# Kernel tuning notes

Hardware: AMD Instinct MI355X
Metric: run time of the kernel (lower is better)

The kernel has to match this reference:

```python
import jax, jax.numpy as jnp
import numpy as np

B, C, H, W = 32, 1, 28, 896
WW = WS = 28
S = (W - WW) // WS + 1  # 32 windows
CONV_DIM, FC_DIM, NUM_CLASSES = 64, 128, 83
FC_IN = CONV_DIM * (H // 2) * (WW // 2)  # 64*14*14 = 12544


def setup_inputs() -> dict:
    key = jax.random.key(0)
    ks = jax.random.split(key, 9)
    sc = 0.05
    return {
        "x": jax.random.normal(ks[0], (B, C, H, W), jnp.float32),
        "conv1_w": jax.random.normal(ks[1], (CONV_DIM, C, 3, 3), jnp.float32) * sc,
        "conv1_b": jax.random.normal(ks[2], (CONV_DIM,), jnp.float32) * sc,
        "conv2_w": jax.random.normal(ks[3], (CONV_DIM, CONV_DIM, 3, 3), jnp.float32) * sc,
        "conv2_b": jax.random.normal(ks[4], (CONV_DIM,), jnp.float32) * sc,
        "fc1_w": jax.random.normal(ks[5], (FC_DIM, FC_IN), jnp.float32) * sc,
        "fc1_b": jax.random.normal(ks[6], (FC_DIM,), jnp.float32) * sc,
        "fc2_w": jax.random.normal(ks[7], (NUM_CLASSES, FC_DIM), jnp.float32) * sc,
        "fc2_b": jax.random.normal(ks[8], (NUM_CLASSES,), jnp.float32) * sc,
    }


def _conv_relu(x, w, b):
    # 3x3 conv, stride 1, padding 1 (torch Conv2d padding=1), then ReLU
    y = jax.lax.conv_general_dilated(
        x, w, window_strides=(1, 1), padding=((1, 1), (1, 1)),
        dimension_numbers=("NCHW", "OIHW", "NCHW"))
    return jax.nn.relu(y + b[None, :, None, None])


def reference(x, conv1_w, conv1_b, conv2_w, conv2_b, fc1_w, fc1_b, fc2_w, fc2_b):
    Bx = x.shape[0]
    # WS == WW -> non-overlapping windows; extract all S windows at once via reshape
    # (B, C, H, S*WW) -> (B*S, C, H, WW)
    win = x.reshape(Bx, C, H, S, WW).transpose(0, 3, 1, 2, 4).reshape(Bx * S, C, H, WW)
    h = _conv_relu(win, conv1_w, conv1_b)
    h = _conv_relu(h, conv2_w, conv2_b)
    # MaxPool2d(2)
    h = jax.lax.reduce_window(h, -jnp.inf, jax.lax.max,
                              window_dimensions=(1, 1, 2, 2),
                              window_strides=(1, 1, 2, 2), padding="VALID")
    # dropout is identity in eval mode
    h = h.reshape(Bx * S, FC_IN)  # torch.flatten(x, 1) on NCHW matches row-major reshape
    h = jax.nn.relu(h @ fc1_w.T + fc1_b)
    logits = h @ fc2_w.T + fc2_b  # (B*S, num_classes)
    # -> (B, num_classes, S) as in the torch module
    return logits.reshape(Bx, S, NUM_CLASSES).transpose(0, 2, 1)
```

## Files before the change

### kernel.cpp

```cpp
#include <hip/hip_runtime.h>
#include <hip/hip_bf16.h>


typedef __attribute__((ext_vector_type(8))) short short8;
typedef __attribute__((ext_vector_type(4))) float f32x4;
typedef __attribute__((ext_vector_type(16))) float f32x16;

#define WB1_E   0u
#define WB2_E   2048u
#define WFC1_E  38912u
#define WFC2_E  1644544u
#define POOL_E  1656832u
#define PART_B  29003776u

__device__ __forceinline__ unsigned short f2bf(float f) {
  unsigned u = __float_as_uint(f);
  u += 0x7fffu + ((u >> 16) & 1u);
  return (unsigned short)(u >> 16);
}
__device__ __forceinline__ unsigned cvtpk_bf16(float a, float b) {
  unsigned r;
  asm("v_cvt_pk_bf16_f32 %0, %1, %2" : "=v"(r) : "v"(a), "v"(b));
  return r;
}

__global__ __launch_bounds__(256) void prep_kernel(
    const float* __restrict__ w1, const float* __restrict__ c1b,
    const float* __restrict__ w2, const float* __restrict__ wfc1,
    const float* __restrict__ wfc2, unsigned short* __restrict__ ws16)
{
  int i = blockIdx.x * blockDim.x + threadIdx.x;
  if (i < 2048) {
    int j = i & 7, l = (i >> 3) & 63, nt = i >> 9;
    int n = nt * 16 + (l & 15), k = 8 * (l >> 4) + j;
    float v = (k < 9) ? w1[n * 9 + k] : (k == 9 ? c1b[n] : 0.f);
    ws16[WB1_E + i] = f2bf(v);
  } else if (i < 38912) {
    int i2 = i - 2048;
    int j = i2 & 7, l = (i2 >> 3) & 63, rest = i2 >> 9;
    int ks = rest % 36, nh = rest / 36;
    int co = nh * 32 + (l & 31);
    int k = ks * 16 + (l >> 5) * 8 + j;
    int dydx = k >> 6, ci = k & 63;
    ws16[WB2_E + i2] = f2bf(w2[co * 576 + ci * 9 + dydx]);
  } else if (i < 1644544) {
    int i2 = i - 38912;
    int j = i2 & 7, l = (i2 >> 3) & 63, rest = i2 >> 9;
    int ks = rest % 392, nt = rest / 392;
    int fcn = nt * 16 + (l & 15);
    int kp = ks * 32 + 8 * (l >> 4) + j;
    int co = kp & 63, r2 = kp >> 6;
    int oxp = r2 % 14, oyp = r2 / 14;
    ws16[WFC1_E + i2] = f2bf(wfc1[fcn * 12544 + co * 196 + oyp * 14 + oxp]);
  } else if (i < 1656832) {
    int i2 = i - 1644544;
    int j = i2 & 7, l = (i2 >> 3) & 63, rest = i2 >> 9;
    int ks = rest & 3, nt = rest >> 2;
    int cls = nt * 16 + (l & 15);
    int k = ks * 32 + 8 * (l >> 4) + j;
    float v = (cls < 83) ? wfc2[cls * 128 + k] : 0.f;
    ws16[WFC2_E + i2] = f2bf(v);
  }
}

__global__ __launch_bounds__(512, 4) void conv_kernel(
    const float* __restrict__ x, const float* __restrict__ c2b,
    unsigned short* __restrict__ ws16)
{
  extern __shared__ char smem[];
  unsigned short* xw = (unsigned short*)(smem + 77760);

  const int tid = threadIdx.x;
  const int wave = tid >> 6, lane = tid & 63;
  const int bid = blockIdx.x;
  const int n = bid >> 1, hf = bid & 1;
  const int rlo = hf ? 15 : 0;
  const int M1 = hf ? 364 : 476;
  const int T1 = hf ? 23 : 30;
  const int lr_off = hf ? -15 : 1;

  const short8* wb1 = (const short8*)(ws16 + WB1_E);
  unsigned short* poolg = ws16 + POOL_E + (unsigned)n * 12544u;

  short8 z8 = {0, 0, 0, 0, 0, 0, 0, 0};
  {
    short8* l8 = (short8*)smem;
    for (int idx = tid; idx < 4860; idx += 512) l8[idx] = z8;
    const float* xg = x + (n >> 5) * 25088 + (n & 31) * 28;
    for (int i = tid; i < 900; i += 512) {
      int yy = (i * 2185) >> 16;
      int xx = i - yy * 30;
      int iy = yy - 1, ix = xx - 1;
      bool inb = (iy >= 0) && (iy < 28) && (ix >= 0) && (ix < 28);
      float v = inb ? xg[iy * 896 + ix] : 0.f;
      xw[i] = f2bf(v);
    }
  }
  __syncthreads();

  {
    const int g = lane >> 4, l15 = lane & 15;
    short8 b1f[4];
#pragma unroll
    for (int nt = 0; nt < 4; ++nt) b1f[nt] = wb1[nt * 64 + lane];
    for (int mt = wave; mt < T1; mt += 8) {
      int m = mt * 16 + l15;
      bool mval = m < M1;
      int mc = mval ? m : M1 - 1;
      int yr = (mc * 2341) >> 16;
      int rr = rlo + yr;
      int ox = mc - yr * 28;
      const char* xb = (const char*)xw + (rr * 30 + ox) * 2;
      short8 a = z8;
      if (g == 0) {
        a[0] = *(const short*)(xb + 0);
        a[1] = *(const short*)(xb + 2);
        a[2] = *(const short*)(xb + 4);
        a[3] = *(const short*)(xb + 60);
        a[4] = *(const short*)(xb + 62);
        a[5] = *(const short*)(xb + 64);
        a[6] = *(const short*)(xb + 120);
        a[7] = *(const short*)(xb + 122);
      } else if (g == 1) {
        a[0] = *(const short*)(xb + 124);
        a[1] = (short)0x3F80;
      }
      f32x4 d[4];
#pragma unroll
      for (int nt = 0; nt < 4; ++nt) {
        f32x4 zz = {0.f, 0.f, 0.f, 0.f};
        d[nt] = __builtin_amdgcn_mfma_f32_16x16x32_bf16(b1f[nt], a, zz, 0, 0, 0);
      }
      if (mval) {
        int spB = ((rr + lr_off) * 30 + ox + 1) * 144;
#pragma unroll
        for (int nt = 0; nt < 4; ++nt) {
          float r0 = fmaxf(d[nt][0], 0.f), r1 = fmaxf(d[nt][1], 0.f);
          float r2 = fmaxf(d[nt][2], 0.f), r3 = fmaxf(d[nt][3], 0.f);
          int co2 = nt * 16 + 4 * g;
          *(unsigned*)(smem + (spB + co2 * 2)) = cvtpk_bf16(r0, r1);
          *(unsigned*)(smem + (spB + co2 * 2 + 4)) = cvtpk_bf16(r2, r3);
        }
      }
    }
  }
  __syncthreads();

  {
    const int l31 = lane & 31;
    const int h = lane >> 5;
    const int T32 = hf ? 11 : 14;
    const int Wh  = hf ? 84 : 112;
    const float bias0 = c2b[l31];
    const float bias1 = c2b[32 + l31];
    const short8* wb2w = (const short8*)(ws16 + WB2_E) + lane;

    const bool v1 = (wave + 8) < T32;
    int baseB0, baseB1;
    {
      int lw = wave * 8 + (l31 >> 2);
      int py = lw / 14, px = lw % 14;
      baseB0 = ((2 * py + ((l31 >> 1) & 1)) * 30 + 2 * px + (l31 & 1)) * 144 + h * 16;
      int tI1 = v1 ? (wave + 8) : wave;
      int lw1 = tI1 * 8 + (l31 >> 2);
      int py1 = lw1 / 14, px1 = lw1 % 14;
      baseB1 = ((2 * py1 + ((l31 >> 1) & 1)) * 30 + 2 * px1 + (l31 & 1)) * 144 + h * 16;
    }
    f32x16 acc00 = (f32x16)(0.0f), acc01 = (f32x16)(0.0f);
    f32x16 acc10 = (f32x16)(0.0f), acc11 = (f32x16)(0.0f);

    short8 bfA0, bfA1, bfA2, bfA3;
    short8 bfB0, bfB1, bfB2, bfB3;

#define LOADB(d0, d1, d2, d3, hp) do {                                   \
      const int ph_ = (hp) >> 1, k0_ = ((hp) & 1) * 2;                   \
      d0 = wb2w[(ph_ * 4 + k0_) * 64];                                   \
      d1 = wb2w[(ph_ * 4 + k0_ + 1) * 64];                               \
      d2 = wb2w[2304 + (ph_ * 4 + k0_) * 64];                            \
      d3 = wb2w[2304 + (ph_ * 4 + k0_ + 1) * 64];                        \
    } while (0)
#define COMPT(hp, base, aL, aH, b0, b1, b2, b3) do {                     \
      const int ph_ = (hp) >> 1, k0_ = ((hp) & 1) * 2;                   \
      const int cell_ = ((ph_ / 3) * 30 + (ph_ % 3)) * 144 + 32 * k0_;   \
      short8 a0 = *(const short8*)(smem + (base + cell_));               \
      short8 a1 = *(const short8*)(smem + (base + cell_ + 32));          \
      aL = __builtin_amdgcn_mfma_f32_32x32x16_bf16(a0, b0, aL, 0, 0, 0); \
      aH = __builtin_amdgcn_mfma_f32_32x32x16_bf16(a0, b2, aH, 0, 0, 0); \
      aL = __builtin_amdgcn_mfma_f32_32x32x16_bf16(a1, b1, aL, 0, 0, 0); \
      aH = __builtin_amdgcn_mfma_f32_32x32x16_bf16(a1, b3, aH, 0, 0, 0); \
    } while (0)

    LOADB(bfA0, bfA1, bfA2, bfA3, 0);
    if (v1) {
#pragma unroll
      for (int hp = 0; hp < 18; hp += 2) {
        __builtin_amdgcn_s_barrier();
        if (hp + 1 < 18) LOADB(bfB0, bfB1, bfB2, bfB3, hp + 1);
        COMPT(hp, baseB0, acc00, acc01, bfA0, bfA1, bfA2, bfA3);
        COMPT(hp, baseB1, acc10, acc11, bfA0, bfA1, bfA2, bfA3);
        if (hp + 2 < 18) LOADB(bfA0, bfA1, bfA2, bfA3, hp + 2);
        COMPT(hp + 1, baseB0, acc00, acc01, bfB0, bfB1, bfB2, bfB3);
        COMPT(hp + 1, baseB1, acc10, acc11, bfB0, bfB1, bfB2, bfB3);
      }
    } else {
#pragma unroll
      for (int hp = 0; hp < 18; hp += 2) {
        __builtin_amdgcn_s_barrier();
        if (hp + 1 < 18) LOADB(bfB0, bfB1, bfB2, bfB3, hp + 1);
        COMPT(hp, baseB0, acc00, acc01, bfA0, bfA1, bfA2, bfA3);
        if (hp + 2 < 18) LOADB(bfA0, bfA1, bfA2, bfA3, hp + 2);
        COMPT(hp + 1, baseB0, acc00, acc01, bfB0, bfB1, bfB2, bfB3);
      }
    }
#undef LOADB
#undef COMPT

#pragma unroll
    for (int q = 0; q < 4; ++q) {
      int lw0 = wave * 8 + 2 * q + h;
      {
        float p0 = fmaxf(fmaxf(acc00[4 * q], acc00[4 * q + 1]),
                         fmaxf(acc00[4 * q + 2], acc00[4 * q + 3]));
        float p1 = fmaxf(fmaxf(acc01[4 * q], acc01[4 * q + 1]),
                         fmaxf(acc01[4 * q + 2], acc01[4 * q + 3]));
        unsigned pk = cvtpk_bf16(fmaxf(p0 + bias0, 0.f), fmaxf(p1 + bias1, 0.f));
        poolg[(hf * 112 + lw0) * 64 + l31]      = (unsigned short)pk;
        poolg[(hf * 112 + lw0) * 64 + 32 + l31] = (unsigned short)(pk >> 16);
      }
      if (v1) {
        int lw1 = (wave + 8) * 8 + 2 * q + h;
        if (lw1 < Wh) {
          float p0 = fmaxf(fmaxf(acc10[4 * q], acc10[4 * q + 1]),
                           fmaxf(acc10[4 * q + 2], acc10[4 * q + 3]));
          float p1 = fmaxf(fmaxf(acc11[4 * q], acc11[4 * q + 1]),
                           fmaxf(acc11[4 * q + 2], acc11[4 * q + 3]));
          unsigned pk = cvtpk_bf16(fmaxf(p0 + bias0, 0.f), fmaxf(p1 + bias1, 0.f));
          poolg[(hf * 112 + lw1) * 64 + l31]      = (unsigned short)pk;
          poolg[(hf * 112 + lw1) * 64 + 32 + l31] = (unsigned short)(pk >> 16);
        }
      }
    }
  }
}

__global__ __launch_bounds__(512) void fc1_kernel(unsigned short* __restrict__ ws16)
{
  extern __shared__ char smem[];
  short8* A8 = (short8*)smem;
  const int tid = threadIdx.x;
  const int wave = tid >> 6, lane = tid & 63;
  const int g = lane >> 4, l15 = lane & 15;
  const int ig = blockIdx.x >> 2, q = blockIdx.x & 3;
  const short8* pool8 = (const short8*)(ws16 + POOL_E);
  const short8* wf1 = (const short8*)(ws16 + WFC1_E);
  {
    int img = tid >> 5, l32 = tid & 31;
    const short8* src = pool8 + (ig * 16 + img) * 1568 + q * 392;
#pragma unroll
    for (int j = 0; j < 13; ++j) {
      int idx = l32 + 32 * j;
      if (idx < 392) A8[img * 393 + idx] = src[idx];
    }
  }
  __syncthreads();
  f32x4 accA = {0.f, 0.f, 0.f, 0.f}, accB = {0.f, 0.f, 0.f, 0.f};
  const short8* wbase = wf1 + (wave * 392 + q * 98) * 64 + lane;
  short8 bP0 = wbase[0 * 64], bP1 = wbase[1 * 64];
  short8 bP2 = wbase[2 * 64], bP3 = wbase[3 * 64];
#pragma unroll 1
  for (int c = 0; c < 24; ++c) {
    int ks = 4 * c;
    short8 a;
    a = A8[l15 * 393 + (ks + 0) * 4 + g];
    accA = __builtin_amdgcn_mfma_f32_16x16x32_bf16(a, bP0, accA, 0, 0, 0);
    bP0 = wbase[(ks + 4) * 64];
    a = A8[l15 * 393 + (ks + 1) * 4 + g];
    accB = __builtin_amdgcn_mfma_f32_16x16x32_bf16(a, bP1, accB, 0, 0, 0);
    bP1 = wbase[(ks + 5) * 64];
    a = A8[l15 * 393 + (ks + 2) * 4 + g];
    accA = __builtin_amdgcn_mfma_f32_16x16x32_bf16(a, bP2, accA, 0, 0, 0);
    bP2 = wbase[(ks + 6) * 64];
    a = A8[l15 * 393 + (ks + 3) * 4 + g];
    accB = __builtin_amdgcn_mfma_f32_16x16x32_bf16(a, bP3, accB, 0, 0, 0);
    bP3 = wbase[(ks + 7) * 64];
  }
  {
    short8 a;
    a = A8[l15 * 393 + 96 * 4 + g];
    accA = __builtin_amdgcn_mfma_f32_16x16x32_bf16(a, bP0, accA, 0, 0, 0);
    a = A8[l15 * 393 + 97 * 4 + g];
    accB = __builtin_amdgcn_mfma_f32_16x16x32_bf16(a, bP1, accB, 0, 0, 0);
  }
  _Float16* part = (_Float16*)((char*)ws16 + PART_B);
  int base = ((q * 64 + ig) * 16 + 4 * g) * 128 + wave * 16 + l15;
#pragma unroll
  for (int i = 0; i < 4; ++i) part[base + i * 128] = (_Float16)(accA[i] + accB[i]);
}

__global__ __launch_bounds__(512) void fc2_kernel(
    const float* __restrict__ b1, const float* __restrict__ b2,
    const unsigned short* __restrict__ ws16, float* __restrict__ out)
{
  __shared__ unsigned short h_s[16 * 136];
  const int tid = threadIdx.x;
  const int wave = tid >> 6, lane = tid & 63;
  const int g = lane >> 4, l15 = lane & 15;
  const int ig = blockIdx.x;
  const _Float16* part = (const _Float16*)((const char*)ws16 + PART_B);
#pragma unroll
  for (int t = 0; t < 4; ++t) {
    int u = tid + 512 * t;
    int img = u >> 7, fcn = u & 127;
    float s = 0.f;
#pragma unroll
    for (int q2 = 0; q2 < 4; ++q2)
      s += (float)part[((q2 * 64 + ig) * 16 + img) * 128 + fcn];
    h_s[img * 136 + fcn] = f2bf(fmaxf(s + b1[fcn], 0.f));
  }
  __syncthreads();
  if (wave < 6) {
    const short8* wf2 = (const short8*)(ws16 + WFC2_E);
    const short8* h8 = (const short8*)h_s;
    f32x4 a2 = {0.f, 0.f, 0.f, 0.f};
#pragma unroll
    for (int ks = 0; ks < 4; ++ks) {
      short8 b = wf2[(wave * 4 + ks) * 64 + lane];
      short8 a = h8[l15 * 17 + ks * 4 + g];
      a2 = __builtin_amdgcn_mfma_f32_16x16x32_bf16(a, b, a2, 0, 0, 0);
    }
    int cls = wave * 16 + l15;
    if (cls < 83) {
      float bias2 = b2[cls];
#pragma unroll
      for (int i = 0; i < 4; ++i) {
        int nimg = ig * 16 + 4 * g + i;
        out[((nimg >> 5) * 83 + cls) * 32 + (nimg & 31)] = a2[i] + bias2;
      }
    }
  }
}

extern "C" void kernel_launch(void* const* d_in, const int* in_sizes, int n_in,
                              void* d_out, int out_size, void* d_ws, size_t ws_size,
                              hipStream_t stream)
{
  const float* x    = (const float*)d_in[0];
  const float* w1   = (const float*)d_in[1];
  const float* c1b  = (const float*)d_in[2];
  const float* w2   = (const float*)d_in[3];
  const float* c2b  = (const float*)d_in[4];
  const float* wfc1 = (const float*)d_in[5];
  const float* bfc1 = (const float*)d_in[6];
  const float* wfc2 = (const float*)d_in[7];
  const float* bfc2 = (const float*)d_in[8];
  unsigned short* ws16 = (unsigned short*)d_ws;
  float* out = (float*)d_out;

  prep_kernel<<<6472, 256, 0, stream>>>(w1, c1b, w2, wfc1, wfc2, ws16);
  conv_kernel<<<2048, 512, 79616, stream>>>(x, c2b, ws16);
  fc1_kernel<<<256, 512, 100608, stream>>>(ws16);
  fc2_kernel<<<64, 512, 0, stream>>>(bfc1, bfc2, ws16, out);
}
```

Before: 95.07 us.

## Split conv work into quarter-image blocks and halve fc1 row tiles

The conv kernel now splits each window image into four pooled-row bands instead of two halves, with a smaller halo-padded LDS buffer and one accumulator tile per wave. The goal is more blocks and higher occupancy (launch bounds 6, about 44KB LDS). The cost is recomputing halo rows of conv1 and leaving idle waves that only join barriers. fc1 now handles 8 images per block across twice as many blocks, with smaller LDS, so half the MFMA rows are wasted duplicates.

```diff
diff --git a/kernel.cpp b/kernel.cpp
--- a/kernel.cpp
+++ b/kernel.cpp
@@ -63,21 +63,26 @@
   }
 }
 
-__global__ __launch_bounds__(512, 4) void conv_kernel(
+__global__ __launch_bounds__(512, 6) void conv_kernel(
     const float* __restrict__ x, const float* __restrict__ c2b,
     unsigned short* __restrict__ ws16)
 {
   extern __shared__ char smem[];
-  unsigned short* xw = (unsigned short*)(smem + 77760);
+  unsigned short* xw = (unsigned short*)(smem + 43200);
 
   const int tid = threadIdx.x;
   const int wave = tid >> 6, lane = tid & 63;
   const int bid = blockIdx.x;
-  const int n = bid >> 1, hf = bid & 1;
-  const int rlo = hf ? 15 : 0;
-  const int M1 = hf ? 364 : 476;
-  const int T1 = hf ? 23 : 30;
-  const int lr_off = hf ? -15 : 1;
+  const int n = bid >> 2, q = bid & 3;
+  const int p0 = (q == 0) ? 0 : (q == 1) ? 4 : (q == 2) ? 8 : 11;
+  const int PR = (q < 2) ? 4 : 3;
+  const int rlo = 2 * p0 - 1;
+  const int rstart = (q == 0) ? 0 : rlo;
+  const int rend = (rlo + 9 < 27) ? rlo + 9 : 27;
+  const int M1 = (rend - rstart + 1) * 28;
+  const int T1 = (M1 + 15) >> 4;
+  const int Wq = PR * 14;
+  const int Tq = (Wq + 7) >> 3;
 
   const short8* wb1 = (const short8*)(ws16 + WB1_E);
   unsigned short* poolg = ws16 + POOL_E + (unsigned)n * 12544u;
@@ -85,12 +90,12 @@
   short8 z8 = {0, 0, 0, 0, 0, 0, 0, 0};
   {
     short8* l8 = (short8*)smem;
-    for (int idx = tid; idx < 4860; idx += 512) l8[idx] = z8;
+    for (int idx = tid; idx < 2700; idx += 512) l8[idx] = z8;
     const float* xg = x + (n >> 5) * 25088 + (n & 31) * 28;
-    for (int i = tid; i < 900; i += 512) {
-      int yy = (i * 2185) >> 16;
-      int xx = i - yy * 30;
-      int iy = yy - 1, ix = xx - 1;
+    for (int i = tid; i < 360; i += 512) {
+      int xr = (i * 2185) >> 16;
+      int xx = i - xr * 30;
+      int iy = rlo - 1 + xr, ix = xx - 1;
       bool inb = (iy >= 0) && (iy < 28) && (ix >= 0) && (ix < 28);
       float v = inb ? xg[iy * 896 + ix] : 0.f;
       xw[i] = f2bf(v);
@@ -108,9 +113,9 @@
       bool mval = m < M1;
       int mc = mval ? m : M1 - 1;
       int yr = (mc * 2341) >> 16;
-      int rr = rlo + yr;
+      int rr = rstart + yr;
       int ox = mc - yr * 28;
-      const char* xb = (const char*)xw + (rr * 30 + ox) * 2;
+      const char* xb = (const char*)xw + ((rr - rlo) * 30 + ox) * 2;
       short8 a = z8;
       if (g == 0) {
         a[0] = *(const short*)(xb + 0);
@@ -132,7 +137,7 @@
         d[nt] = __builtin_amdgcn_mfma_f32_16x16x32_bf16(b1f[nt], a, zz, 0, 0, 0);
       }
       if (mval) {
-        int spB = ((rr + lr_off) * 30 + ox + 1) * 144;
+        int spB = ((rr - rlo) * 30 + ox + 1) * 144;
 #pragma unroll
         for (int nt = 0; nt < 4; ++nt) {
           float r0 = fmaxf(d[nt][0], 0.f), r1 = fmaxf(d[nt][1], 0.f);
@@ -149,28 +154,20 @@
   {
     const int l31 = lane & 31;
     const int h = lane >> 5;
-    const int T32 = hf ? 11 : 14;
-    const int Wh  = hf ? 84 : 112;
+    const bool real = wave < Tq;
+    const int tile = real ? wave : 0;
     const float bias0 = c2b[l31];
     const float bias1 = c2b[32 + l31];
     const short8* wb2w = (const short8*)(ws16 + WB2_E) + lane;
 
-    const bool v1 = (wave + 8) < T32;
-    int baseB0, baseB1;
-    {
-      int lw = wave * 8 + (l31 >> 2);
-      int py = lw / 14, px = lw % 14;
-      baseB0 = ((2 * py + ((l31 >> 1) & 1)) * 30 + 2 * px + (l31 & 1)) * 144 + h * 16;
-      int tI1 = v1 ? (wave + 8) : wave;
-      int lw1 = tI1 * 8 + (l31 >> 2);
-      int py1 = lw1 / 14, px1 = lw1 % 14;
-      baseB1 = ((2 * py1 + ((l31 >> 1) & 1)) * 30 + 2 * px1 + (l31 & 1)) * 144 + h * 16;
-    }
-    f32x16 acc00 = (f32x16)(0.0f), acc01 = (f32x16)(0.0f);
-    f32x16 acc10 = (f32x16)(0.0f), acc11 = (f32x16)(0.0f);
-
-    short8 bfA0, bfA1, bfA2, bfA3;
-    short8 bfB0, bfB1, bfB2, bfB3;
+    int lwl = tile * 8 + (l31 >> 2);
+    if (lwl >= Wq) lwl = Wq - 1;
+    int pyl = (lwl * 2341) >> 15;
+    int pxl = lwl - pyl * 14;
+    int p = l31 & 3;
+    const int baseB = ((2 * pyl + (p >> 1)) * 30 + 2 * pxl + (p & 1)) * 144 + h * 16;
+
+    f32x16 acc0 = (f32x16)(0.0f), acc1 = (f32x16)(0.0f);
 
 #define LOADB(d0, d1, d2, d3, hp) do {                                   \
       const int ph_ = (hp) >> 1, k0_ = ((hp) & 1) * 2;                   \
@@ -179,64 +176,50 @@
       d2 = wb2w[2304 + (ph_ * 4 + k0_) * 64];                            \
       d3 = wb2w[2304 + (ph_ * 4 + k0_ + 1) * 64];                        \
     } while (0)
-#define COMPT(hp, base, aL, aH, b0, b1, b2, b3) do {                     \
+#define COMPT(hp, b0, b1, b2, b3) do {                                   \
       const int ph_ = (hp) >> 1, k0_ = ((hp) & 1) * 2;                   \
       const int cell_ = ((ph_ / 3) * 30 + (ph_ % 3)) * 144 + 32 * k0_;   \
-      short8 a0 = *(const short8*)(smem + (base + cell_));               \
-      short8 a1 = *(const short8*)(smem + (base + cell_ + 32));          \
-      aL = __builtin_amdgcn_mfma_f32_32x32x16_bf16(a0, b0, aL, 0, 0, 0); \
-      aH = __builtin_amdgcn_mfma_f32_32x32x16_bf16(a0, b2, aH, 0, 0, 0); \
-      aL = __builtin_amdgcn_mfma_f32_32x32x16_bf16(a1, b1, aL, 0, 0, 0); \
-      aH = __builtin_amdgcn_mfma_f32_32x32x16_bf16(a1, b3, aH, 0, 0, 0); \
+      short8 a0 = *(const short8*)(smem + (baseB + cell_));              \
+      short8 a1 = *(const short8*)(smem + (baseB + cell_ + 32));         \
+      acc0 = __builtin_amdgcn_mfma_f32_32x32x16_bf16(a0, b0, acc0, 0, 0, 0); \
+      acc1 = __builtin_amdgcn_mfma_f32_32x32x16_bf16(a0, b2, acc1, 0, 0, 0); \
+      acc0 = __builtin_amdgcn_mfma_f32_32x32x16_bf16(a1, b1, acc0, 0, 0, 0); \
+      acc1 = __builtin_amdgcn_mfma_f32_32x32x16_bf16(a1, b3, acc1, 0, 0, 0); \
     } while (0)
 
-    LOADB(bfA0, bfA1, bfA2, bfA3, 0);
-    if (v1) {
+    if (real) {
+      short8 bfA0, bfA1, bfA2, bfA3, bfB0, bfB1, bfB2, bfB3;
+      LOADB(bfA0, bfA1, bfA2, bfA3, 0);
 #pragma unroll
       for (int hp = 0; hp < 18; hp += 2) {
         __builtin_amdgcn_s_barrier();
-        if (hp + 1 < 18) LOADB(bfB0, bfB1, bfB2, bfB3, hp + 1);
-        COMPT(hp, baseB0, acc00, acc01, bfA0, bfA1, bfA2, bfA3);
-        COMPT(hp, baseB1, acc10, acc11, bfA0, bfA1, bfA2, bfA3);
+        LOADB(bfB0, bfB1, bfB2, bfB3, hp + 1);
+        COMPT(hp, bfA0, bfA1, bfA2, bfA3);
         if (hp + 2 < 18) LOADB(bfA0, bfA1, bfA2, bfA3, hp + 2);
-        COMPT(hp + 1, baseB0, acc00, acc01, bfB0, bfB1, bfB2, bfB3);
-        COMPT(hp + 1, baseB1, acc10, acc11, bfB0, bfB1, bfB2, bfB3);
+        COMPT(hp + 1, bfB0, bfB1, bfB2, bfB3);
       }
     } else {
 #pragma unroll
-      for (int hp = 0; hp < 18; hp += 2) {
-        __builtin_amdgcn_s_barrier();
-        if (hp + 1 < 18) LOADB(bfB0, bfB1, bfB2, bfB3, hp + 1);
-        COMPT(hp, baseB0, acc00, acc01, bfA0, bfA1, bfA2, bfA3);
-        if (hp + 2 < 18) LOADB(bfA0, bfA1, bfA2, bfA3, hp + 2);
-        COMPT(hp + 1, baseB0, acc00, acc01, bfB0, bfB1, bfB2, bfB3);
-      }
+      for (int it = 0; it < 9; ++it) __builtin_amdgcn_s_barrier();
     }
 #undef LOADB
 #undef COMPT
 
-#pragma unroll
-    for (int q = 0; q < 4; ++q) {
-      int lw0 = wave * 8 + 2 * q + h;
-      {
-        float p0 = fmaxf(fmaxf(acc00[4 * q], acc00[4 * q + 1]),
-                         fmaxf(acc00[4 * q + 2], acc00[4 * q + 3]));
-        float p1 = fmaxf(fmaxf(acc01[4 * q], acc01[4 * q + 1]),
-                         fmaxf(acc01[4 * q + 2], acc01[4 * q + 3]));
-        unsigned pk = cvtpk_bf16(fmaxf(p0 + bias0, 0.f), fmaxf(p1 + bias1, 0.f));
-        poolg[(hf * 112 + lw0) * 64 + l31]      = (unsigned short)pk;
-        poolg[(hf * 112 + lw0) * 64 + 32 + l31] = (unsigned short)(pk >> 16);
-      }
-      if (v1) {
-        int lw1 = (wave + 8) * 8 + 2 * q + h;
-        if (lw1 < Wh) {
-          float p0 = fmaxf(fmaxf(acc10[4 * q], acc10[4 * q + 1]),
-                           fmaxf(acc10[4 * q + 2], acc10[4 * q + 3]));
-          float p1 = fmaxf(fmaxf(acc11[4 * q], acc11[4 * q + 1]),
-                           fmaxf(acc11[4 * q + 2], acc11[4 * q + 3]));
-          unsigned pk = cvtpk_bf16(fmaxf(p0 + bias0, 0.f), fmaxf(p1 + bias1, 0.f));
-          poolg[(hf * 112 + lw1) * 64 + l31]      = (unsigned short)pk;
-          poolg[(hf * 112 + lw1) * 64 + 32 + l31] = (unsigned short)(pk >> 16);
+    if (real) {
+#pragma unroll
+      for (int rq = 0; rq < 4; ++rq) {
+        int lwq = wave * 8 + 2 * rq + h;
+        if (lwq < Wq) {
+          float p0v = fmaxf(fmaxf(acc0[4 * rq], acc0[4 * rq + 1]),
+                            fmaxf(acc0[4 * rq + 2], acc0[4 * rq + 3]));
+          float p1v = fmaxf(fmaxf(acc1[4 * rq], acc1[4 * rq + 1]),
+                            fmaxf(acc1[4 * rq + 2], acc1[4 * rq + 3]));
+          unsigned pk = cvtpk_bf16(fmaxf(p0v + bias0, 0.f), fmaxf(p1v + bias1, 0.f));
+          int py2 = (lwq * 2341) >> 15;
+          int px2 = lwq - py2 * 14;
+          int row = ((p0 + py2) * 14 + px2) * 64;
+          poolg[row + l31]      = (unsigned short)pk;
+          poolg[row + 32 + l31] = (unsigned short)(pk >> 16);
         }
       }
     }
@@ -250,51 +233,54 @@
   const int tid = threadIdx.x;
   const int wave = tid >> 6, lane = tid & 63;
   const int g = lane >> 4, l15 = lane & 15;
-  const int ig = blockIdx.x >> 2, q = blockIdx.x & 3;
+  const int ig2 = blockIdx.x >> 2, q = blockIdx.x & 3;
   const short8* pool8 = (const short8*)(ws16 + POOL_E);
   const short8* wf1 = (const short8*)(ws16 + WFC1_E);
   {
-    int img = tid >> 5, l32 = tid & 31;
-    const short8* src = pool8 + (ig * 16 + img) * 1568 + q * 392;
-#pragma unroll
-    for (int j = 0; j < 13; ++j) {
-      int idx = l32 + 32 * j;
+    int img = tid >> 6, l64 = tid & 63;
+    const short8* src = pool8 + (ig2 * 8 + img) * 1568 + q * 392;
+#pragma unroll
+    for (int j = 0; j < 7; ++j) {
+      int idx = l64 + 64 * j;
       if (idx < 392) A8[img * 393 + idx] = src[idx];
     }
   }
   __syncthreads();
   f32x4 accA = {0.f, 0.f, 0.f, 0.f}, accB = {0.f, 0.f, 0.f, 0.f};
   const short8* wbase = wf1 + (wave * 392 + q * 98) * 64 + lane;
+  const int arow = (l15 & 7) * 393;
   short8 bP0 = wbase[0 * 64], bP1 = wbase[1 * 64];
   short8 bP2 = wbase[2 * 64], bP3 = wbase[3 * 64];
 #pragma unroll 1
   for (int c = 0; c < 24; ++c) {
     int ks = 4 * c;
     short8 a;
-    a = A8[l15 * 393 + (ks + 0) * 4 + g];
+    a = A8[arow + (ks + 0) * 4 + g];
     accA = __builtin_amdgcn_mfma_f32_16x16x32_bf16(a, bP0, accA, 0, 0, 0);
     bP0 = wbase[(ks + 4) * 64];
-    a = A8[l15 * 393 + (ks + 1) * 4 + g];
+    a = A8[arow + (ks + 1) * 4 + g];
     accB = __builtin_amdgcn_mfma_f32_16x16x32_bf16(a, bP1, accB, 0, 0, 0);
     bP1 = wbase[(ks + 5) * 64];
-    a = A8[l15 * 393 + (ks + 2) * 4 + g];
+    a = A8[arow + (ks + 2) * 4 + g];
     accA = __builtin_amdgcn_mfma_f32_16x16x32_bf16(a, bP2, accA, 0, 0, 0);
     bP2 = wbase[(ks + 6) * 64];
-    a = A8[l15 * 393 + (ks + 3) * 4 + g];
+    a = A8[arow + (ks + 3) * 4 + g];
     accB = __builtin_amdgcn_mfma_f32_16x16x32_bf16(a, bP3, accB, 0, 0, 0);
     bP3 = wbase[(ks + 7) * 64];
   }
   {
     short8 a;
-    a = A8[l15 * 393 + 96 * 4 + g];
+    a = A8[arow + 96 * 4 + g];
     accA = __builtin_amdgcn_mfma_f32_16x16x32_bf16(a, bP0, accA, 0, 0, 0);
-    a = A8[l15 * 393 + 97 * 4 + g];
+    a = A8[arow + 97 * 4 + g];
     accB = __builtin_amdgcn_mfma_f32_16x16x32_bf16(a, bP1, accB, 0, 0, 0);
   }
-  _Float16* part = (_Float16*)((char*)ws16 + PART_B);
-  int base = ((q * 64 + ig) * 16 + 4 * g) * 128 + wave * 16 + l15;
-#pragma unroll
-  for (int i = 0; i < 4; ++i) part[base + i * 128] = (_Float16)(accA[i] + accB[i]);
+  if (g < 2) {
+    _Float16* part = (_Float16*)((char*)ws16 + PART_B);
+    int base = ((q * 128 + ig2) * 8 + 4 * g) * 128 + wave * 16 + l15;
+#pragma unroll
+    for (int i = 0; i < 4; ++i) part[base + i * 128] = (_Float16)(accA[i] + accB[i]);
+  }
 }
 
 __global__ __launch_bounds__(512) void fc2_kernel(
@@ -311,10 +297,11 @@
   for (int t = 0; t < 4; ++t) {
     int u = tid + 512 * t;
     int img = u >> 7, fcn = u & 127;
+    int ig2 = ig * 2 + (img >> 3), img8 = img & 7;
     float s = 0.f;
 #pragma unroll
     for (int q2 = 0; q2 < 4; ++q2)
-      s += (float)part[((q2 * 64 + ig) * 16 + img) * 128 + fcn];
+      s += (float)part[((q2 * 128 + ig2) * 8 + img8) * 128 + fcn];
     h_s[img * 136 + fcn] = f2bf(fmaxf(s + b1[fcn], 0.f));
   }
   __syncthreads();
@@ -357,7 +344,7 @@
   float* out = (float*)d_out;
 
   prep_kernel<<<6472, 256, 0, stream>>>(w1, c1b, w2, wfc1, wfc2, ws16);
-  conv_kernel<<<2048, 512, 79616, stream>>>(x, c2b, ws16);
-  fc1_kernel<<<256, 512, 100608, stream>>>(ws16);
+  conv_kernel<<<4096, 512, 43920, stream>>>(x, c2b, ws16);
+  fc1_kernel<<<512, 512, 50304, stream>>>(ws16);
   fc2_kernel<<<64, 512, 0, stream>>>(bfc1, bfc2, ws16, out);
 }
```

New measurement: 111.2 us. +16.9%, slower.

## Halve conv block to four waves, each computing up to four conv2 tiles

Applied to the files above, without the earlier changes.

The conv kernel now launches 256 threads instead of 512, and each wave accumulates up to four 32-row conv2 output tiles instead of two. Every conv2 weight fragment loaded from global memory is therefore reused across more MFMA tiles per wave. The per-wave base-address arithmetic is reworked, with clamping and a cheaper divide by 14. The cost is more accumulator registers (eight f32x16) and fewer waves per block to hide LDS and global latency, while LDS use per block stays about the same.

```diff
diff --git a/kernel.cpp b/kernel.cpp
--- a/kernel.cpp
+++ b/kernel.cpp
@@ -63,7 +63,7 @@
   }
 }
 
-__global__ __launch_bounds__(512, 4) void conv_kernel(
+__global__ __launch_bounds__(256, 2) void conv_kernel(
     const float* __restrict__ x, const float* __restrict__ c2b,
     unsigned short* __restrict__ ws16)
 {
@@ -85,9 +85,9 @@
   short8 z8 = {0, 0, 0, 0, 0, 0, 0, 0};
   {
     short8* l8 = (short8*)smem;
-    for (int idx = tid; idx < 4860; idx += 512) l8[idx] = z8;
+    for (int idx = tid; idx < 4860; idx += 256) l8[idx] = z8;
     const float* xg = x + (n >> 5) * 25088 + (n & 31) * 28;
-    for (int i = tid; i < 900; i += 512) {
+    for (int i = tid; i < 900; i += 256) {
       int yy = (i * 2185) >> 16;
       int xx = i - yy * 30;
       int iy = yy - 1, ix = xx - 1;
@@ -103,7 +103,7 @@
     short8 b1f[4];
 #pragma unroll
     for (int nt = 0; nt < 4; ++nt) b1f[nt] = wb1[nt * 64 + lane];
-    for (int mt = wave; mt < T1; mt += 8) {
+    for (int mt = wave; mt < T1; mt += 4) {
       int m = mt * 16 + l15;
       bool mval = m < M1;
       int mc = mval ? m : M1 - 1;
@@ -155,19 +155,23 @@
     const float bias1 = c2b[32 + l31];
     const short8* wb2w = (const short8*)(ws16 + WB2_E) + lane;
 
-    const bool v1 = (wave + 8) < T32;
-    int baseB0, baseB1;
-    {
-      int lw = wave * 8 + (l31 >> 2);
-      int py = lw / 14, px = lw % 14;
-      baseB0 = ((2 * py + ((l31 >> 1) & 1)) * 30 + 2 * px + (l31 & 1)) * 144 + h * 16;
-      int tI1 = v1 ? (wave + 8) : wave;
-      int lw1 = tI1 * 8 + (l31 >> 2);
-      int py1 = lw1 / 14, px1 = lw1 % 14;
-      baseB1 = ((2 * py1 + ((l31 >> 1) & 1)) * 30 + 2 * px1 + (l31 & 1)) * 144 + h * 16;
-    }
-    f32x16 acc00 = (f32x16)(0.0f), acc01 = (f32x16)(0.0f);
-    f32x16 acc10 = (f32x16)(0.0f), acc11 = (f32x16)(0.0f);
+    const bool v2 = (wave + 8) < T32;
+    const bool v3 = (wave + 12) < T32;
+    int baseB[4];
+#pragma unroll
+    for (int t = 0; t < 4; ++t) {
+      int tI = wave + 4 * t;
+      int lw = tI * 8 + (l31 >> 2);
+      if (lw > Wh - 1) lw = Wh - 1;
+      int py = (lw * 2341) >> 15;
+      int px = lw - py * 14;
+      int p = l31 & 3;
+      baseB[t] = ((2 * py + (p >> 1)) * 30 + 2 * px + (p & 1)) * 144 + h * 16;
+    }
+    f32x16 a00 = (f32x16)(0.0f), a01 = (f32x16)(0.0f);
+    f32x16 a10 = (f32x16)(0.0f), a11 = (f32x16)(0.0f);
+    f32x16 a20 = (f32x16)(0.0f), a21 = (f32x16)(0.0f);
+    f32x16 a30 = (f32x16)(0.0f), a31 = (f32x16)(0.0f);
 
     short8 bfA0, bfA1, bfA2, bfA3;
     short8 bfB0, bfB1, bfB2, bfB3;
@@ -182,64 +186,56 @@
 #define COMPT(hp, base, aL, aH, b0, b1, b2, b3) do {                     \
       const int ph_ = (hp) >> 1, k0_ = ((hp) & 1) * 2;                   \
       const int cell_ = ((ph_ / 3) * 30 + (ph_ % 3)) * 144 + 32 * k0_;   \
-      short8 a0 = *(const short8*)(smem + (base + cell_));               \
-      short8 a1 = *(const short8*)(smem + (base + cell_ + 32));          \
-      aL = __builtin_amdgcn_mfma_f32_32x32x16_bf16(a0, b0, aL, 0, 0, 0); \
-      aH = __builtin_amdgcn_mfma_f32_32x32x16_bf16(a0, b2, aH, 0, 0, 0); \
-      aL = __builtin_amdgcn_mfma_f32_32x32x16_bf16(a1, b1, aL, 0, 0, 0); \
-      aH = __builtin_amdgcn_mfma_f32_32x32x16_bf16(a1, b3, aH, 0, 0, 0); \
+      short8 x0 = *(const short8*)(smem + (base + cell_));               \
+      short8 x1 = *(const short8*)(smem + (base + cell_ + 32));          \
+      aL = __builtin_amdgcn_mfma_f32_32x32x16_bf16(x0, b0, aL, 0, 0, 0); \
+      aH = __builtin_amdgcn_mfma_f32_32x32x16_bf16(x0, b2, aH, 0, 0, 0); \
+      aL = __builtin_amdgcn_mfma_f32_32x32x16_bf16(x1, b1, aL, 0, 0, 0); \
+      aH = __builtin_amdgcn_mfma_f32_32x32x16_bf16(x1, b3, aH, 0, 0, 0); \
     } while (0)
+#define COMP4(hp, b0, b1, b2, b3) do {                                   \
+      COMPT(hp, baseB[0], a00, a01, b0, b1, b2, b3);                     \
+      COMPT(hp, baseB[1], a10, a11, b0, b1, b2, b3);                     \
+      if (v2) COMPT(hp, baseB[2], a20, a21, b0, b1, b2, b3);             \
+      if (v3) COMPT(hp, baseB[3], a30, a31, b0, b1, b2, b3);             \
+    } while (0)
 
     LOADB(bfA0, bfA1, bfA2, bfA3, 0);
-    if (v1) {
-#pragma unroll
-      for (int hp = 0; hp < 18; hp += 2) {
-        __builtin_amdgcn_s_barrier();
-        if (hp + 1 < 18) LOADB(bfB0, bfB1, bfB2, bfB3, hp + 1);
-        COMPT(hp, baseB0, acc00, acc01, bfA0, bfA1, bfA2, bfA3);
-        COMPT(hp, baseB1, acc10, acc11, bfA0, bfA1, bfA2, bfA3);
-        if (hp + 2 < 18) LOADB(bfA0, bfA1, bfA2, bfA3, hp + 2);
-        COMPT(hp + 1, baseB0, acc00, acc01, bfB0, bfB1, bfB2, bfB3);
-        COMPT(hp + 1, baseB1, acc10, acc11, bfB0, bfB1, bfB2, bfB3);
-      }
-    } else {
-#pragma unroll
-      for (int hp = 0; hp < 18; hp += 2) {
-        __builtin_amdgcn_s_barrier();
-        if (hp + 1 < 18) LOADB(bfB0, bfB1, bfB2, bfB3, hp + 1);
-        COMPT(hp, baseB0, acc00, acc01, bfA0, bfA1, bfA2, bfA3);
-        if (hp + 2 < 18) LOADB(bfA0, bfA1, bfA2, bfA3, hp + 2);
-        COMPT(hp + 1, baseB0, acc00, acc01, bfB0, bfB1, bfB2, bfB3);
-      }
+#pragma unroll
+    for (int hp = 0; hp < 18; hp += 2) {
+      __builtin_amdgcn_s_barrier();
+      LOADB(bfB0, bfB1, bfB2, bfB3, hp + 1);
+      COMP4(hp, bfA0, bfA1, bfA2, bfA3);
+      if (hp + 2 < 18) LOADB(bfA0, bfA1, bfA2, bfA3, hp + 2);
+      COMP4(hp + 1, bfB0, bfB1, bfB2, bfB3);
     }
 #undef LOADB
 #undef COMPT
-
-#pragma unroll
-    for (int q = 0; q < 4; ++q) {
-      int lw0 = wave * 8 + 2 * q + h;
-      {
-        float p0 = fmaxf(fmaxf(acc00[4 * q], acc00[4 * q + 1]),
-                         fmaxf(acc00[4 * q + 2], acc00[4 * q + 3]));
-        float p1 = fmaxf(fmaxf(acc01[4 * q], acc01[4 * q + 1]),
-                         fmaxf(acc01[4 * q + 2], acc01[4 * q + 3]));
-        unsigned pk = cvtpk_bf16(fmaxf(p0 + bias0, 0.f), fmaxf(p1 + bias1, 0.f));
-        poolg[(hf * 112 + lw0) * 64 + l31]      = (unsigned short)pk;
-        poolg[(hf * 112 + lw0) * 64 + 32 + l31] = (unsigned short)(pk >> 16);
-      }
-      if (v1) {
-        int lw1 = (wave + 8) * 8 + 2 * q + h;
-        if (lw1 < Wh) {
-          float p0 = fmaxf(fmaxf(acc10[4 * q], acc10[4 * q + 1]),
-                           fmaxf(acc10[4 * q + 2], acc10[4 * q + 3]));
-          float p1 = fmaxf(fmaxf(acc11[4 * q], acc11[4 * q + 1]),
-                           fmaxf(acc11[4 * q + 2], acc11[4 * q + 3]));
-          unsigned pk = cvtpk_bf16(fmaxf(p0 + bias0, 0.f), fmaxf(p1 + bias1, 0.f));
-          poolg[(hf * 112 + lw1) * 64 + l31]      = (unsigned short)pk;
-          poolg[(hf * 112 + lw1) * 64 + 32 + l31] = (unsigned short)(pk >> 16);
-        }
-      }
-    }
+#undef COMP4
+
+#define STORE_T(t, aL, aH) do {                                          \
+      int tI = wave + 4 * (t);                                           \
+      _Pragma("unroll")                                                  \
+      for (int rq = 0; rq < 4; ++rq) {                                   \
+        int lwq = tI * 8 + 2 * rq + h;                                   \
+        if (lwq < Wh) {                                                  \
+          float p0v = fmaxf(fmaxf(aL[4 * rq], aL[4 * rq + 1]),           \
+                            fmaxf(aL[4 * rq + 2], aL[4 * rq + 3]));      \
+          float p1v = fmaxf(fmaxf(aH[4 * rq], aH[4 * rq + 1]),           \
+                            fmaxf(aH[4 * rq + 2], aH[4 * rq + 3]));      \
+          unsigned pk = cvtpk_bf16(fmaxf(p0v + bias0, 0.f),              \
+                                   fmaxf(p1v + bias1, 0.f));             \
+          int row = (hf * 112 + lwq) * 64;                               \
+          poolg[row + l31]      = (unsigned short)pk;                    \
+          poolg[row + 32 + l31] = (unsigned short)(pk >> 16);            \
+        }                                                                \
+      }                                                                  \
+    } while (0)
+    STORE_T(0, a00, a01);
+    STORE_T(1, a10, a11);
+    if (v2) STORE_T(2, a20, a21);
+    if (v3) STORE_T(3, a30, a31);
+#undef STORE_T
   }
 }
 
@@ -357,7 +353,7 @@
   float* out = (float*)d_out;
 
   prep_kernel<<<6472, 256, 0, stream>>>(w1, c1b, w2, wfc1, wfc2, ws16);
-  conv_kernel<<<2048, 512, 79616, stream>>>(x, c2b, ws16);
+  conv_kernel<<<2048, 256, 79560, stream>>>(x, c2b, ws16);
   fc1_kernel<<<256, 512, 100608, stream>>>(ws16);
   fc2_kernel<<<64, 512, 0, stream>>>(bfc1, bfc2, ws16, out);
 }
```

Result: slower. 97.97 us (+3.1%).

## Overlap FC weight conversion with conv kernel and raise MFMA wave priority

Applied to the files above, without the earlier changes.

Conversion of the large fc1/fc2 weights to bf16 moves out of the prep kernel and into 256 extra blocks appended to the conv kernel grid, so this memory-bound work can overlap the compute-bound conv blocks instead of running serially before them. The prep kernel shrinks to the small conv-weight work. s_setprio is also raised around the MFMA sections of the conv inner loop to favour compute issue. The extra blocks use the same large LDS allocation as the conv blocks, which can reduce occupancy while they are resident, and because they are scheduled last they may run after most of the conv work rather than alongside it.

```diff
diff --git a/kernel.cpp b/kernel.cpp
--- a/kernel.cpp
+++ b/kernel.cpp
@@ -26,8 +26,7 @@
 
 __global__ __launch_bounds__(256) void prep_kernel(
     const float* __restrict__ w1, const float* __restrict__ c1b,
-    const float* __restrict__ w2, const float* __restrict__ wfc1,
-    const float* __restrict__ wfc2, unsigned short* __restrict__ ws16)
+    const float* __restrict__ w2, unsigned short* __restrict__ ws16)
 {
   int i = blockIdx.x * blockDim.x + threadIdx.x;
   if (i < 2048) {
@@ -43,36 +42,46 @@
     int k = ks * 16 + (l >> 5) * 8 + j;
     int dydx = k >> 6, ci = k & 63;
     ws16[WB2_E + i2] = f2bf(w2[co * 576 + ci * 9 + dydx]);
-  } else if (i < 1644544) {
-    int i2 = i - 38912;
-    int j = i2 & 7, l = (i2 >> 3) & 63, rest = i2 >> 9;
-    int ks = rest % 392, nt = rest / 392;
-    int fcn = nt * 16 + (l & 15);
-    int kp = ks * 32 + 8 * (l >> 4) + j;
-    int co = kp & 63, r2 = kp >> 6;
-    int oxp = r2 % 14, oyp = r2 / 14;
-    ws16[WFC1_E + i2] = f2bf(wfc1[fcn * 12544 + co * 196 + oyp * 14 + oxp]);
-  } else if (i < 1656832) {
-    int i2 = i - 1644544;
-    int j = i2 & 7, l = (i2 >> 3) & 63, rest = i2 >> 9;
-    int ks = rest & 3, nt = rest >> 2;
-    int cls = nt * 16 + (l & 15);
-    int k = ks * 32 + 8 * (l >> 4) + j;
-    float v = (cls < 83) ? wfc2[cls * 128 + k] : 0.f;
-    ws16[WFC2_E + i2] = f2bf(v);
   }
 }
 
 __global__ __launch_bounds__(512, 4) void conv_kernel(
     const float* __restrict__ x, const float* __restrict__ c2b,
+    const float* __restrict__ wfc1, const float* __restrict__ wfc2,
     unsigned short* __restrict__ ws16)
 {
   extern __shared__ char smem[];
+  const int tid = threadIdx.x;
+  const int bid = blockIdx.x;
+
+  if (bid >= 2048) {
+    for (unsigned u = (unsigned)(bid - 2048) * 512u + tid; u < 1617920u;
+         u += 131072u) {
+      if (u < 1605632u) {
+        unsigned i2 = u;
+        int j = i2 & 7, l = (i2 >> 3) & 63;
+        unsigned rest = i2 >> 9;
+        int ks = rest % 392, nt = rest / 392;
+        int fcn = nt * 16 + (l & 15);
+        int kp = ks * 32 + 8 * (l >> 4) + j;
+        int co = kp & 63, r2 = kp >> 6;
+        int oxp = r2 % 14, oyp = r2 / 14;
+        ws16[WFC1_E + i2] = f2bf(wfc1[fcn * 12544 + co * 196 + oyp * 14 + oxp]);
+      } else {
+        unsigned i2 = u - 1605632u;
+        int j = i2 & 7, l = (i2 >> 3) & 63, rest = i2 >> 9;
+        int ks = rest & 3, nt = rest >> 2;
+        int cls = nt * 16 + (l & 15);
+        int k = ks * 32 + 8 * (l >> 4) + j;
+        float v = (cls < 83) ? wfc2[cls * 128 + k] : 0.f;
+        ws16[WFC2_E + i2] = f2bf(v);
+      }
+    }
+    return;
+  }
+
   unsigned short* xw = (unsigned short*)(smem + 77760);
-
-  const int tid = threadIdx.x;
   const int wave = tid >> 6, lane = tid & 63;
-  const int bid = blockIdx.x;
   const int n = bid >> 1, hf = bid & 1;
   const int rlo = hf ? 15 : 0;
   const int M1 = hf ? 364 : 476;
@@ -196,20 +205,28 @@
       for (int hp = 0; hp < 18; hp += 2) {
         __builtin_amdgcn_s_barrier();
         if (hp + 1 < 18) LOADB(bfB0, bfB1, bfB2, bfB3, hp + 1);
+        __builtin_amdgcn_s_setprio(1);
         COMPT(hp, baseB0, acc00, acc01, bfA0, bfA1, bfA2, bfA3);
         COMPT(hp, baseB1, acc10, acc11, bfA0, bfA1, bfA2, bfA3);
+        __builtin_amdgcn_s_setprio(0);
         if (hp + 2 < 18) LOADB(bfA0, bfA1, bfA2, bfA3, hp + 2);
+        __builtin_amdgcn_s_setprio(1);
         COMPT(hp + 1, baseB0, acc00, acc01, bfB0, bfB1, bfB2, bfB3);
         COMPT(hp + 1, baseB1, acc10, acc11, bfB0, bfB1, bfB2, bfB3);
+        __builtin_amdgcn_s_setprio(0);
       }
     } else {
 #pragma unroll
       for (int hp = 0; hp < 18; hp += 2) {
         __builtin_amdgcn_s_barrier();
         if (hp + 1 < 18) LOADB(bfB0, bfB1, bfB2, bfB3, hp + 1);
+        __builtin_amdgcn_s_setprio(1);
         COMPT(hp, baseB0, acc00, acc01, bfA0, bfA1, bfA2, bfA3);
+        __builtin_amdgcn_s_setprio(0);
         if (hp + 2 < 18) LOADB(bfA0, bfA1, bfA2, bfA3, hp + 2);
+        __builtin_amdgcn_s_setprio(1);
         COMPT(hp + 1, baseB0, acc00, acc01, bfB0, bfB1, bfB2, bfB3);
+        __builtin_amdgcn_s_setprio(0);
       }
     }
 #undef LOADB
@@ -356,8 +373,8 @@
   unsigned short* ws16 = (unsigned short*)d_ws;
   float* out = (float*)d_out;
 
-  prep_kernel<<<6472, 256, 0, stream>>>(w1, c1b, w2, wfc1, wfc2, ws16);
-  conv_kernel<<<2048, 512, 79616, stream>>>(x, c2b, ws16);
+  prep_kernel<<<152, 256, 0, stream>>>(w1, c1b, w2, ws16);
+  conv_kernel<<<2304, 512, 79616, stream>>>(x, c2b, wfc1, wfc2, ws16);
   fc1_kernel<<<256, 512, 100608, stream>>>(ws16);
   fc2_kernel<<<64, 512, 0, stream>>>(bfc1, bfc2, ws16, out);
 }
```

Measured after the change: 96.57 us. Within noise of the previous version (+1.6%).
